# Kernel tuning notes

Measured on AMD Instinct MI355X. Metric: run time of the kernel, lower is better.

Reference implementation:

```python
import jax, jax.numpy as jnp
import numpy as np

N_NODES = 50000   # num graph nodes
N_EDGES = 800000  # avg degree 16
D = 96            # in_channels == out_channels (residual aggr_out + x)


def setup_inputs() -> dict:
    key = jax.random.key(0)
    k0, k1, k2, k3, k4 = jax.random.split(key, 5)
    x = jax.random.normal(k0, (N_NODES, D), dtype=jnp.float32)
    edge_index = jax.random.randint(k1, (2, N_EDGES), 0, N_NODES)  # [2,E]: row0=src(j), row1=dst(i)
    edge_weight = jax.random.uniform(k2, (N_EDGES,), dtype=jnp.float32)
    pagerank = jax.random.uniform(k3, (N_NODES,), dtype=jnp.float32)
    # nn.Linear(in_channels, out_channels) params
    W = jax.random.normal(k4, (D, D), dtype=jnp.float32) / np.sqrt(D).astype(np.float32)
    b = jnp.zeros((D,), dtype=jnp.float32)
    return {"x": x, "edge_index": edge_index, "edge_weight": edge_weight,
            "pagerank": pagerank, "W": W, "b": b}


def reference(x, edge_index, edge_weight, pagerank, W, b):
    # CGCConv (PyG MessagePassing, aggr='add', flow source_to_target):
    #   message: edge_weight * x_j * pagerank_j   (gather from source nodes)
    #   aggregate: scatter-add to destination nodes
    #   update: Linear(aggr_out + x)
    src = edge_index[0]
    dst = edge_index[1]
    # [E, D] messages: per-edge gather-multiply
    msgs = edge_weight[:, None] * x[src] * pagerank[src][:, None]
    aggr = jax.ops.segment_sum(msgs, dst, num_segments=x.shape[0])  # [N, D]
    return (aggr + x) @ W.T + b
```

## Files before the change

kernel.cpp:

```cpp
#include <hip/hip_runtime.h>


constexpr int NN = 50000;
constexpr int NE = 800000;
constexpr int DD = 96;
constexpr int NB = 196;
constexpr int EPB = 2048;
constexpr int NBLK = (NE + EPB - 1) / EPB;
constexpr int CAPB = 4608;

__device__ inline unsigned short f2bf(float f) {
    unsigned u = __float_as_uint(f);
    return (unsigned short)((u + 0x7FFFu + ((u >> 16) & 1u)) >> 16);
}

__global__ __launch_bounds__(256) void k_cvt(const float4* __restrict__ x4,
                                             ushort4* __restrict__ y16v,
                                             int* __restrict__ cur1) {
    if (blockIdx.x == 0 && threadIdx.x < NB) cur1[threadIdx.x] = 0;
    int i = blockIdx.x * blockDim.x + threadIdx.x;
    if (i < NN * DD / 4) {
        float4 v = x4[i];
        y16v[i] = make_ushort4(f2bf(v.x), f2bf(v.y), f2bf(v.z), f2bf(v.w));
    }
}

__global__ __launch_bounds__(256) void k_binA(const int* __restrict__ src,
                                              const int* __restrict__ dst,
                                              const float* __restrict__ ew,
                                              const float* __restrict__ pr,
                                              int* __restrict__ cur1,
                                              int2* __restrict__ stage) {
    __shared__ int h[NB];
    __shared__ int gb[NB];
    int tid = threadIdx.x;
    for (int i = tid; i < NB; i += 256) h[i] = 0;
    __syncthreads();
    int base = blockIdx.x * EPB;

    int2 ent[8]; int bkt[8]; int lrk[8];
    #pragma unroll
    for (int j = 0; j < 8; j++) {
        int e = base + j * 256 + tid;
        bkt[j] = -1;
        if (e < NE) {
            int d = dst[e];
            int s = src[e];
            float c = ew[e] * pr[s];
            int b = d >> 8;
            bkt[j] = b;
            lrk[j] = atomicAdd(&h[b], 1);
            ent[j] = make_int2(s | ((d & 255) << 16), __float_as_int(c));
        }
    }
    __syncthreads();
    for (int i = tid; i < NB; i += 256)
        gb[i] = h[i] ? atomicAdd(&cur1[i], h[i]) : 0;
    __syncthreads();
    #pragma unroll
    for (int j = 0; j < 8; j++)
        if (bkt[j] >= 0)
            stage[(size_t)bkt[j] * CAPB + gb[bkt[j]] + lrk[j]] = ent[j];
}

__global__ __launch_bounds__(512) void k_sortB(int2* __restrict__ stage,
                                               const int* __restrict__ cur1,
                                               int* __restrict__ offs,
                                               int* __restrict__ counts) {
    __shared__ int h[256];
    __shared__ int sc[256];
    __shared__ int2 sorted[CAPB];
    int b = blockIdx.x;
    int tid = threadIdx.x;
    size_t base = (size_t)b * CAPB;
    int n = cur1[b];

    for (int i = tid; i < 256; i += 512) h[i] = 0;
    __syncthreads();

    int2 ent[9]; int lrk[9];
    int m = 0;
    for (int i = tid; i < n; i += 512) {
        int2 e = stage[base + i];
        int dloc = (e.x >> 16) & 0xff;
        lrk[m] = atomicAdd(&h[dloc], 1);
        ent[m] = e;
        m++;
    }
    __syncthreads();
    if (tid < 256) sc[tid] = h[tid];
    __syncthreads();
    #pragma unroll
    for (int o = 1; o < 256; o <<= 1) {
        int t = 0;
        if (tid < 256 && tid >= o) t = sc[tid - o];
        __syncthreads();
        if (tid < 256) sc[tid] += t;
        __syncthreads();
    }
    m = 0;
    for (int i = tid; i < n; i += 512) {
        int2 e = ent[m];
        int dloc = (e.x >> 16) & 0xff;
        sorted[sc[dloc] - h[dloc] + lrk[m]] = e;
        m++;
    }
    __syncthreads();
    for (int i = tid; i < n; i += 512) stage[base + i] = sorted[i];
    if (tid < 256) {
        int d = (b << 8) + tid;
        if (d < NN) {
            offs[d] = (int)base + sc[tid] - h[tid];
            counts[d] = h[tid];
        }
    }
}

__global__ __launch_bounds__(256) void k_pull(const ushort4* __restrict__ y16v,
                                              const float4* __restrict__ x4,
                                              const int* __restrict__ offs,
                                              const int* __restrict__ counts,
                                              const int2* __restrict__ ep,
                                              float4* __restrict__ out4) {
    int g = blockIdx.x * 8 + (threadIdx.x >> 5);
    int lane = threadIdx.x & 31;
    if (g >= NN || lane >= 24) return;
    int beg = offs[g];
    int deg = counts[g];
    float ax = 0.f, ay = 0.f, az = 0.f, aw = 0.f;
    int k = 0;
    for (; k + 4 <= deg; k += 4) {
        int2 e0 = ep[beg + k];
        int2 e1 = ep[beg + k + 1];
        int2 e2 = ep[beg + k + 2];
        int2 e3 = ep[beg + k + 3];
        ushort4 u0 = y16v[(size_t)(e0.x & 0xffff) * 24 + lane];
        ushort4 u1 = y16v[(size_t)(e1.x & 0xffff) * 24 + lane];
        ushort4 u2 = y16v[(size_t)(e2.x & 0xffff) * 24 + lane];
        ushort4 u3 = y16v[(size_t)(e3.x & 0xffff) * 24 + lane];
        float c0 = __int_as_float(e0.y), c1 = __int_as_float(e1.y);
        float c2 = __int_as_float(e2.y), c3 = __int_as_float(e3.y);
        ax += c0 * __uint_as_float((unsigned)u0.x << 16)
            + c1 * __uint_as_float((unsigned)u1.x << 16)
            + c2 * __uint_as_float((unsigned)u2.x << 16)
            + c3 * __uint_as_float((unsigned)u3.x << 16);
        ay += c0 * __uint_as_float((unsigned)u0.y << 16)
            + c1 * __uint_as_float((unsigned)u1.y << 16)
            + c2 * __uint_as_float((unsigned)u2.y << 16)
            + c3 * __uint_as_float((unsigned)u3.y << 16);
        az += c0 * __uint_as_float((unsigned)u0.z << 16)
            + c1 * __uint_as_float((unsigned)u1.z << 16)
            + c2 * __uint_as_float((unsigned)u2.z << 16)
            + c3 * __uint_as_float((unsigned)u3.z << 16);
        aw += c0 * __uint_as_float((unsigned)u0.w << 16)
            + c1 * __uint_as_float((unsigned)u1.w << 16)
            + c2 * __uint_as_float((unsigned)u2.w << 16)
            + c3 * __uint_as_float((unsigned)u3.w << 16);
    }
    for (; k < deg; k++) {
        int2 e = ep[beg + k];
        ushort4 u = y16v[(size_t)(e.x & 0xffff) * 24 + lane];
        float c = __int_as_float(e.y);
        ax += c * __uint_as_float((unsigned)u.x << 16);
        ay += c * __uint_as_float((unsigned)u.y << 16);
        az += c * __uint_as_float((unsigned)u.z << 16);
        aw += c * __uint_as_float((unsigned)u.w << 16);
    }
    float4 xn = x4[(size_t)g * 24 + lane];
    out4[(size_t)g * 24 + lane] = make_float4(ax + xn.x, ay + xn.y,
                                              az + xn.z, aw + xn.w);
}

constexpr int SWS = 100;
__global__ __launch_bounds__(256, 4) void k_gemm(float* __restrict__ io,
                                                 const float* __restrict__ W,
                                                 const float* __restrict__ b) {
    __shared__ float sWt[DD * SWS];
    int tid = threadIdx.x;
    for (int i = tid; i < DD * DD; i += 256) {
        int o = i / DD, d = i - o * DD;
        sWt[d * SWS + o] = W[i];
    }
    __syncthreads();

    int wave = tid >> 6, lane = tid & 63;
    int og = lane & 7, rgl = lane >> 3;
    int o0 = og * 12;
    int rbase = blockIdx.x * 128 + wave * 32 + rgl;
    const float4* io4 = (const float4*)io;

    int r[4];
    #pragma unroll
    for (int t = 0; t < 4; t++) {
        int rr = rbase + 8 * t;
        r[t] = (rr < NN) ? rr : (NN - 1);
    }

    float acc[4][12];
    #pragma unroll
    for (int t = 0; t < 4; t++)
        #pragma unroll
        for (int m = 0; m < 12; m++) acc[t][m] = 0.f;

    for (int d4 = 0; d4 < 24; d4++) {
        float4 xv[4];
        #pragma unroll
        for (int t = 0; t < 4; t++) xv[t] = io4[(size_t)r[t] * 24 + d4];
        #pragma unroll
        for (int dj = 0; dj < 4; dj++) {
            const float* wp = &sWt[(d4 * 4 + dj) * SWS + o0];
            float4 w0 = *(const float4*)(wp);
            float4 w1 = *(const float4*)(wp + 4);
            float4 w2 = *(const float4*)(wp + 8);
            #pragma unroll
            for (int t = 0; t < 4; t++) {
                float xs = (dj == 0) ? xv[t].x : (dj == 1) ? xv[t].y
                         : (dj == 2) ? xv[t].z : xv[t].w;
                acc[t][0]  += xs * w0.x;  acc[t][1]  += xs * w0.y;
                acc[t][2]  += xs * w0.z;  acc[t][3]  += xs * w0.w;
                acc[t][4]  += xs * w1.x;  acc[t][5]  += xs * w1.y;
                acc[t][6]  += xs * w1.z;  acc[t][7]  += xs * w1.w;
                acc[t][8]  += xs * w2.x;  acc[t][9]  += xs * w2.y;
                acc[t][10] += xs * w2.z;  acc[t][11] += xs * w2.w;
            }
        }
    }

    float4 b0 = *(const float4*)(b + o0);
    float4 b1 = *(const float4*)(b + o0 + 4);
    float4 b2 = *(const float4*)(b + o0 + 8);
    float4* io4w = (float4*)io;
    #pragma unroll
    for (int t = 0; t < 4; t++) {
        int rr = rbase + 8 * t;
        if (rr < NN) {
            size_t base = (size_t)rr * 24 + og * 3;
            io4w[base + 0] = make_float4(acc[t][0] + b0.x, acc[t][1] + b0.y,
                                         acc[t][2] + b0.z, acc[t][3] + b0.w);
            io4w[base + 1] = make_float4(acc[t][4] + b1.x, acc[t][5] + b1.y,
                                         acc[t][6] + b1.z, acc[t][7] + b1.w);
            io4w[base + 2] = make_float4(acc[t][8] + b2.x, acc[t][9] + b2.y,
                                         acc[t][10] + b2.z, acc[t][11] + b2.w);
        }
    }
}

extern "C" void kernel_launch(void* const* d_in, const int* in_sizes, int n_in,
                              void* d_out, int out_size, void* d_ws, size_t ws_size,
                              hipStream_t stream) {
    const float* x  = (const float*)d_in[0];
    const int*   ei = (const int*)d_in[1];
    const float* ew = (const float*)d_in[2];
    const float* pr = (const float*)d_in[3];
    const float* W  = (const float*)d_in[4];
    const float* b  = (const float*)d_in[5];
    float* out = (float*)d_out;

    int2* stage = (int2*)d_ws;
    unsigned short* y16 = (unsigned short*)(stage + (size_t)NB * CAPB);
    int* cur1   = (int*)(y16 + (size_t)NN * DD);
    int* offs   = cur1 + NB;
    int* counts = offs + NN;

    const int* src = ei;
    const int* dst = ei + NE;

    int n4 = NN * DD / 4;
    k_cvt<<<(n4 + 255) / 256, 256, 0, stream>>>((const float4*)x, (ushort4*)y16, cur1);
    k_binA<<<NBLK, 256, 0, stream>>>(src, dst, ew, pr, cur1, stage);
    k_sortB<<<NB, 512, 0, stream>>>(stage, cur1, offs, counts);
    k_pull<<<(NN + 7) / 8, 256, 0, stream>>>((const ushort4*)y16, (const float4*)x,
                                             offs, counts, stage, (float4*)out);
    k_gemm<<<(NN + 127) / 128, 256, 0, stream>>>(out, W, b);
}
```

Before: 166.6 us.

## Fuse bucket sort with neighbor pull and merge bf16 convert into binning

Bucket width drops from 256 to 128 destination nodes, so each per-bucket sort can keep its sorted edges in shared memory and do the gather-accumulate directly from there. This removes the write-back of sorted edges, the offs/counts arrays and one kernel launch. The x-to-bf16 conversion now runs in extra blocks of the binning kernel, and a tiny zeroing kernel resets the counters. The cost is that the pull phase runs on only 391 blocks, each with 8 wave groups of 64 lanes (48 active), which may leave the GPU under-occupied and serialize the gather latency.

```diff
diff --git a/kernel.cpp b/kernel.cpp
--- a/kernel.cpp
+++ b/kernel.cpp
@@ -4,57 +4,63 @@
 constexpr int NN = 50000;
 constexpr int NE = 800000;
 constexpr int DD = 96;
-constexpr int NB = 196;
-constexpr int EPB = 2048;
+constexpr int NB = 391;
+constexpr int CAPB = 2432;
+constexpr int EPB = 4096;
 constexpr int NBLK = (NE + EPB - 1) / EPB;
-constexpr int CAPB = 4608;
+constexpr int NCVT = (NN * DD / 4 + 511) / 512;
 
 __device__ inline unsigned short f2bf(float f) {
     unsigned u = __float_as_uint(f);
     return (unsigned short)((u + 0x7FFFu + ((u >> 16) & 1u)) >> 16);
 }
-
-__global__ __launch_bounds__(256) void k_cvt(const float4* __restrict__ x4,
-                                             ushort4* __restrict__ y16v,
-                                             int* __restrict__ cur1) {
-    if (blockIdx.x == 0 && threadIdx.x < NB) cur1[threadIdx.x] = 0;
-    int i = blockIdx.x * blockDim.x + threadIdx.x;
-    if (i < NN * DD / 4) {
-        float4 v = x4[i];
-        y16v[i] = make_ushort4(f2bf(v.x), f2bf(v.y), f2bf(v.z), f2bf(v.w));
-    }
-}
-
-__global__ __launch_bounds__(256) void k_binA(const int* __restrict__ src,
+__device__ inline float bfh(unsigned short v) {
+    return __uint_as_float((unsigned)v << 16);
+}
+
+__global__ __launch_bounds__(512) void k_zero(int* __restrict__ cur1) {
+    if (threadIdx.x < NB) cur1[threadIdx.x] = 0;
+}
+
+__global__ __launch_bounds__(512) void k_prep(const int* __restrict__ src,
                                               const int* __restrict__ dst,
                                               const float* __restrict__ ew,
                                               const float* __restrict__ pr,
                                               int* __restrict__ cur1,
-                                              int2* __restrict__ stage) {
+                                              int2* __restrict__ stage,
+                                              const float4* __restrict__ x4,
+                                              ushort4* __restrict__ y16v) {
+    int tid = threadIdx.x;
+    if (blockIdx.x >= NBLK) {
+        int i = (blockIdx.x - NBLK) * 512 + tid;
+        if (i < NN * DD / 4) {
+            float4 v = x4[i];
+            y16v[i] = make_ushort4(f2bf(v.x), f2bf(v.y), f2bf(v.z), f2bf(v.w));
+        }
+        return;
+    }
     __shared__ int h[NB];
     __shared__ int gb[NB];
-    int tid = threadIdx.x;
-    for (int i = tid; i < NB; i += 256) h[i] = 0;
+    for (int i = tid; i < NB; i += 512) h[i] = 0;
     __syncthreads();
     int base = blockIdx.x * EPB;
 
     int2 ent[8]; int bkt[8]; int lrk[8];
     #pragma unroll
     for (int j = 0; j < 8; j++) {
-        int e = base + j * 256 + tid;
+        int e = base + j * 512 + tid;
         bkt[j] = -1;
         if (e < NE) {
             int d = dst[e];
             int s = src[e];
             float c = ew[e] * pr[s];
-            int b = d >> 8;
-            bkt[j] = b;
-            lrk[j] = atomicAdd(&h[b], 1);
-            ent[j] = make_int2(s | ((d & 255) << 16), __float_as_int(c));
-        }
-    }
-    __syncthreads();
-    for (int i = tid; i < NB; i += 256)
+            bkt[j] = d >> 7;
+            lrk[j] = atomicAdd(&h[d >> 7], 1);
+            ent[j] = make_int2(s | ((d & 127) << 16), __float_as_int(c));
+        }
+    }
+    __syncthreads();
+    for (int i = tid; i < NB; i += 512)
         gb[i] = h[i] ? atomicAdd(&cur1[i], h[i]) : 0;
     __syncthreads();
     #pragma unroll
@@ -63,112 +69,85 @@
             stage[(size_t)bkt[j] * CAPB + gb[bkt[j]] + lrk[j]] = ent[j];
 }
 
-__global__ __launch_bounds__(512) void k_sortB(int2* __restrict__ stage,
-                                               const int* __restrict__ cur1,
-                                               int* __restrict__ offs,
-                                               int* __restrict__ counts) {
-    __shared__ int h[256];
-    __shared__ int sc[256];
-    __shared__ int2 sorted[CAPB];
-    int b = blockIdx.x;
-    int tid = threadIdx.x;
+__global__ __launch_bounds__(512) void k_sortpull(const int2* __restrict__ stage,
+                                                  const int* __restrict__ cur1,
+                                                  const ushort2* __restrict__ y2,
+                                                  const float2* __restrict__ x2,
+                                                  float2* __restrict__ out2) {
+    __shared__ int2 es[CAPB];
+    __shared__ int h[128];
+    __shared__ int sc[128];
+    int b = blockIdx.x, tid = threadIdx.x;
     size_t base = (size_t)b * CAPB;
     int n = cur1[b];
 
-    for (int i = tid; i < 256; i += 512) h[i] = 0;
-    __syncthreads();
-
-    int2 ent[9]; int lrk[9];
+    if (tid < 128) h[tid] = 0;
+    __syncthreads();
+    int2 ent[5]; int lrk[5];
     int m = 0;
     for (int i = tid; i < n; i += 512) {
         int2 e = stage[base + i];
-        int dloc = (e.x >> 16) & 0xff;
-        lrk[m] = atomicAdd(&h[dloc], 1);
-        ent[m] = e;
-        m++;
-    }
-    __syncthreads();
-    if (tid < 256) sc[tid] = h[tid];
-    __syncthreads();
-    #pragma unroll
-    for (int o = 1; o < 256; o <<= 1) {
+        lrk[m] = atomicAdd(&h[(e.x >> 16) & 127], 1);
+        ent[m] = e; m++;
+    }
+    __syncthreads();
+    if (tid < 128) sc[tid] = h[tid];
+    __syncthreads();
+    #pragma unroll
+    for (int o = 1; o < 128; o <<= 1) {
         int t = 0;
-        if (tid < 256 && tid >= o) t = sc[tid - o];
+        if (tid < 128 && tid >= o) t = sc[tid - o];
         __syncthreads();
-        if (tid < 256) sc[tid] += t;
+        if (tid < 128) sc[tid] += t;
         __syncthreads();
     }
     m = 0;
     for (int i = tid; i < n; i += 512) {
         int2 e = ent[m];
-        int dloc = (e.x >> 16) & 0xff;
-        sorted[sc[dloc] - h[dloc] + lrk[m]] = e;
+        int dl = (e.x >> 16) & 127;
+        es[sc[dl] - h[dl] + lrk[m]] = e;
         m++;
     }
     __syncthreads();
-    for (int i = tid; i < n; i += 512) stage[base + i] = sorted[i];
-    if (tid < 256) {
-        int d = (b << 8) + tid;
-        if (d < NN) {
-            offs[d] = (int)base + sc[tid] - h[tid];
-            counts[d] = h[tid];
-        }
-    }
-}
-
-__global__ __launch_bounds__(256) void k_pull(const ushort4* __restrict__ y16v,
-                                              const float4* __restrict__ x4,
-                                              const int* __restrict__ offs,
-                                              const int* __restrict__ counts,
-                                              const int2* __restrict__ ep,
-                                              float4* __restrict__ out4) {
-    int g = blockIdx.x * 8 + (threadIdx.x >> 5);
-    int lane = threadIdx.x & 31;
-    if (g >= NN || lane >= 24) return;
-    int beg = offs[g];
-    int deg = counts[g];
-    float ax = 0.f, ay = 0.f, az = 0.f, aw = 0.f;
-    int k = 0;
-    for (; k + 4 <= deg; k += 4) {
-        int2 e0 = ep[beg + k];
-        int2 e1 = ep[beg + k + 1];
-        int2 e2 = ep[beg + k + 2];
-        int2 e3 = ep[beg + k + 3];
-        ushort4 u0 = y16v[(size_t)(e0.x & 0xffff) * 24 + lane];
-        ushort4 u1 = y16v[(size_t)(e1.x & 0xffff) * 24 + lane];
-        ushort4 u2 = y16v[(size_t)(e2.x & 0xffff) * 24 + lane];
-        ushort4 u3 = y16v[(size_t)(e3.x & 0xffff) * 24 + lane];
-        float c0 = __int_as_float(e0.y), c1 = __int_as_float(e1.y);
-        float c2 = __int_as_float(e2.y), c3 = __int_as_float(e3.y);
-        ax += c0 * __uint_as_float((unsigned)u0.x << 16)
-            + c1 * __uint_as_float((unsigned)u1.x << 16)
-            + c2 * __uint_as_float((unsigned)u2.x << 16)
-            + c3 * __uint_as_float((unsigned)u3.x << 16);
-        ay += c0 * __uint_as_float((unsigned)u0.y << 16)
-            + c1 * __uint_as_float((unsigned)u1.y << 16)
-            + c2 * __uint_as_float((unsigned)u2.y << 16)
-            + c3 * __uint_as_float((unsigned)u3.y << 16);
-        az += c0 * __uint_as_float((unsigned)u0.z << 16)
-            + c1 * __uint_as_float((unsigned)u1.z << 16)
-            + c2 * __uint_as_float((unsigned)u2.z << 16)
-            + c3 * __uint_as_float((unsigned)u3.z << 16);
-        aw += c0 * __uint_as_float((unsigned)u0.w << 16)
-            + c1 * __uint_as_float((unsigned)u1.w << 16)
-            + c2 * __uint_as_float((unsigned)u2.w << 16)
-            + c3 * __uint_as_float((unsigned)u3.w << 16);
-    }
-    for (; k < deg; k++) {
-        int2 e = ep[beg + k];
-        ushort4 u = y16v[(size_t)(e.x & 0xffff) * 24 + lane];
-        float c = __int_as_float(e.y);
-        ax += c * __uint_as_float((unsigned)u.x << 16);
-        ay += c * __uint_as_float((unsigned)u.y << 16);
-        az += c * __uint_as_float((unsigned)u.z << 16);
-        aw += c * __uint_as_float((unsigned)u.w << 16);
-    }
-    float4 xn = x4[(size_t)g * 24 + lane];
-    out4[(size_t)g * 24 + lane] = make_float4(ax + xn.x, ay + xn.y,
-                                              az + xn.z, aw + xn.w);
+
+    int grp = tid >> 6, lane = tid & 63;
+    for (int ni = grp; ni < 128; ni += 8) {
+        int d = (b << 7) + ni;
+        if (d >= NN) break;
+        int beg = sc[ni] - h[ni];
+        int deg = h[ni];
+        float a0 = 0.f, a1 = 0.f;
+        int k = 0;
+        for (; k + 4 <= deg; k += 4) {
+            int2 e0 = es[beg + k],     e1 = es[beg + k + 1];
+            int2 e2 = es[beg + k + 2], e3 = es[beg + k + 3];
+            if (lane < 48) {
+                ushort2 u0 = y2[(size_t)(e0.x & 0xffff) * 48 + lane];
+                ushort2 u1 = y2[(size_t)(e1.x & 0xffff) * 48 + lane];
+                ushort2 u2 = y2[(size_t)(e2.x & 0xffff) * 48 + lane];
+                ushort2 u3 = y2[(size_t)(e3.x & 0xffff) * 48 + lane];
+                float c0 = __int_as_float(e0.y), c1 = __int_as_float(e1.y);
+                float c2 = __int_as_float(e2.y), c3 = __int_as_float(e3.y);
+                a0 += c0 * bfh(u0.x) + c1 * bfh(u1.x)
+                    + c2 * bfh(u2.x) + c3 * bfh(u3.x);
+                a1 += c0 * bfh(u0.y) + c1 * bfh(u1.y)
+                    + c2 * bfh(u2.y) + c3 * bfh(u3.y);
+            }
+        }
+        for (; k < deg; k++) {
+            int2 e = es[beg + k];
+            if (lane < 48) {
+                ushort2 u = y2[(size_t)(e.x & 0xffff) * 48 + lane];
+                float c = __int_as_float(e.y);
+                a0 += c * bfh(u.x);
+                a1 += c * bfh(u.y);
+            }
+        }
+        if (lane < 48) {
+            float2 xv = x2[(size_t)d * 48 + lane];
+            out2[(size_t)d * 48 + lane] = make_float2(a0 + xv.x, a1 + xv.y);
+        }
+    }
 }
 
 constexpr int SWS = 100;
@@ -258,18 +237,15 @@
 
     int2* stage = (int2*)d_ws;
     unsigned short* y16 = (unsigned short*)(stage + (size_t)NB * CAPB);
-    int* cur1   = (int*)(y16 + (size_t)NN * DD);
-    int* offs   = cur1 + NB;
-    int* counts = offs + NN;
+    int* cur1 = (int*)(y16 + (size_t)NN * DD);
 
     const int* src = ei;
     const int* dst = ei + NE;
 
-    int n4 = NN * DD / 4;
-    k_cvt<<<(n4 + 255) / 256, 256, 0, stream>>>((const float4*)x, (ushort4*)y16, cur1);
-    k_binA<<<NBLK, 256, 0, stream>>>(src, dst, ew, pr, cur1, stage);
-    k_sortB<<<NB, 512, 0, stream>>>(stage, cur1, offs, counts);
-    k_pull<<<(NN + 7) / 8, 256, 0, stream>>>((const ushort4*)y16, (const float4*)x,
-                                             offs, counts, stage, (float4*)out);
+    k_zero<<<1, 512, 0, stream>>>(cur1);
+    k_prep<<<NBLK + NCVT, 512, 0, stream>>>(src, dst, ew, pr, cur1, stage,
+                                            (const float4*)x, (ushort4*)y16);
+    k_sortpull<<<NB, 512, 0, stream>>>(stage, cur1, (const ushort2*)y16,
+                                       (const float2*)x, (float2*)out);
     k_gemm<<<(NN + 127) / 128, 256, 0, stream>>>(out, W, b);
 }
```

Result: slower. 194.4 us (+16.7%).

## Fuse bf16 conversion into binning kernel, add nontemporal edge traffic and deeper pull unroll

Applied to the files above, without the earlier changes.

The separate x-to-bf16 conversion kernel is merged into the binning kernel as extra blocks, with a tiny kernel now zeroing the bucket counters. Binning blocks grow to 512 threads and 4096 edges each. Edge records become 64-bit words moved with nontemporal loads and stores. The pull loop gains an 8-way unrolled path that issues more independent gathers in flight. The goal is fewer launch gaps, less cache pollution from the streamed edge data, and more memory-level parallelism, at the cost of higher register use and an extra tiny launch.

```diff
diff --git a/kernel.cpp b/kernel.cpp
--- a/kernel.cpp
+++ b/kernel.cpp
@@ -5,71 +5,82 @@
 constexpr int NE = 800000;
 constexpr int DD = 96;
 constexpr int NB = 196;
-constexpr int EPB = 2048;
+constexpr int CAPB = 4608;
+constexpr int EPB = 4096;
 constexpr int NBLK = (NE + EPB - 1) / EPB;
-constexpr int CAPB = 4608;
+constexpr int NCVT = (NN * DD / 4 + 511) / 512;
 
 __device__ inline unsigned short f2bf(float f) {
     unsigned u = __float_as_uint(f);
     return (unsigned short)((u + 0x7FFFu + ((u >> 16) & 1u)) >> 16);
 }
-
-__global__ __launch_bounds__(256) void k_cvt(const float4* __restrict__ x4,
-                                             ushort4* __restrict__ y16v,
-                                             int* __restrict__ cur1) {
-    if (blockIdx.x == 0 && threadIdx.x < NB) cur1[threadIdx.x] = 0;
-    int i = blockIdx.x * blockDim.x + threadIdx.x;
-    if (i < NN * DD / 4) {
-        float4 v = x4[i];
-        y16v[i] = make_ushort4(f2bf(v.x), f2bf(v.y), f2bf(v.z), f2bf(v.w));
-    }
-}
-
-__global__ __launch_bounds__(256) void k_binA(const int* __restrict__ src,
+__device__ inline float bfh(unsigned short v) {
+    return __uint_as_float((unsigned)v << 16);
+}
+__device__ inline unsigned long long pack_e(int meta, float c) {
+    return (unsigned long long)(unsigned)meta |
+           ((unsigned long long)(unsigned)__float_as_uint(c) << 32);
+}
+
+__global__ __launch_bounds__(256) void k_zero(int* __restrict__ cur1) {
+    if (threadIdx.x < NB) cur1[threadIdx.x] = 0;
+}
+
+__global__ __launch_bounds__(512) void k_prep(const int* __restrict__ src,
                                               const int* __restrict__ dst,
                                               const float* __restrict__ ew,
                                               const float* __restrict__ pr,
                                               int* __restrict__ cur1,
-                                              int2* __restrict__ stage) {
+                                              unsigned long long* __restrict__ stage,
+                                              const float4* __restrict__ x4,
+                                              ushort4* __restrict__ y16v) {
+    int tid = threadIdx.x;
+    if (blockIdx.x >= NBLK) {
+        int i = (blockIdx.x - NBLK) * 512 + tid;
+        if (i < NN * DD / 4) {
+            float4 v = x4[i];
+            y16v[i] = make_ushort4(f2bf(v.x), f2bf(v.y), f2bf(v.z), f2bf(v.w));
+        }
+        return;
+    }
     __shared__ int h[NB];
     __shared__ int gb[NB];
-    int tid = threadIdx.x;
-    for (int i = tid; i < NB; i += 256) h[i] = 0;
+    for (int i = tid; i < NB; i += 512) h[i] = 0;
     __syncthreads();
     int base = blockIdx.x * EPB;
 
-    int2 ent[8]; int bkt[8]; int lrk[8];
+    unsigned long long ent[8]; int bkt[8]; int lrk[8];
     #pragma unroll
     for (int j = 0; j < 8; j++) {
-        int e = base + j * 256 + tid;
+        int e = base + j * 512 + tid;
         bkt[j] = -1;
         if (e < NE) {
             int d = dst[e];
             int s = src[e];
             float c = ew[e] * pr[s];
-            int b = d >> 8;
-            bkt[j] = b;
-            lrk[j] = atomicAdd(&h[b], 1);
-            ent[j] = make_int2(s | ((d & 255) << 16), __float_as_int(c));
-        }
-    }
-    __syncthreads();
-    for (int i = tid; i < NB; i += 256)
+            bkt[j] = d >> 8;
+            lrk[j] = atomicAdd(&h[d >> 8], 1);
+            ent[j] = pack_e(s | ((d & 255) << 16), c);
+        }
+    }
+    __syncthreads();
+    for (int i = tid; i < NB; i += 512)
         gb[i] = h[i] ? atomicAdd(&cur1[i], h[i]) : 0;
     __syncthreads();
     #pragma unroll
     for (int j = 0; j < 8; j++)
         if (bkt[j] >= 0)
-            stage[(size_t)bkt[j] * CAPB + gb[bkt[j]] + lrk[j]] = ent[j];
-}
-
-__global__ __launch_bounds__(512) void k_sortB(int2* __restrict__ stage,
+            __builtin_nontemporal_store(
+                ent[j], &stage[(size_t)bkt[j] * CAPB + gb[bkt[j]] + lrk[j]]);
+}
+
+__global__ __launch_bounds__(512) void k_sortB(unsigned long long* __restrict__ stage,
                                                const int* __restrict__ cur1,
                                                int* __restrict__ offs,
                                                int* __restrict__ counts) {
     __shared__ int h[256];
     __shared__ int sc[256];
-    __shared__ int2 sorted[CAPB];
+    __shared__ unsigned long long sorted[CAPB];
     int b = blockIdx.x;
     int tid = threadIdx.x;
     size_t base = (size_t)b * CAPB;
@@ -78,11 +89,11 @@
     for (int i = tid; i < 256; i += 512) h[i] = 0;
     __syncthreads();
 
-    int2 ent[9]; int lrk[9];
+    unsigned long long ent[9]; int lrk[9];
     int m = 0;
     for (int i = tid; i < n; i += 512) {
-        int2 e = stage[base + i];
-        int dloc = (e.x >> 16) & 0xff;
+        unsigned long long e = __builtin_nontemporal_load(&stage[base + i]);
+        int dloc = ((int)e >> 16) & 0xff;
         lrk[m] = atomicAdd(&h[dloc], 1);
         ent[m] = e;
         m++;
@@ -100,13 +111,14 @@
     }
     m = 0;
     for (int i = tid; i < n; i += 512) {
-        int2 e = ent[m];
-        int dloc = (e.x >> 16) & 0xff;
+        unsigned long long e = ent[m];
+        int dloc = ((int)e >> 16) & 0xff;
         sorted[sc[dloc] - h[dloc] + lrk[m]] = e;
         m++;
     }
     __syncthreads();
-    for (int i = tid; i < n; i += 512) stage[base + i] = sorted[i];
+    for (int i = tid; i < n; i += 512)
+        __builtin_nontemporal_store(sorted[i], &stage[base + i]);
     if (tid < 256) {
         int d = (b << 8) + tid;
         if (d < NN) {
@@ -120,7 +132,7 @@
                                               const float4* __restrict__ x4,
                                               const int* __restrict__ offs,
                                               const int* __restrict__ counts,
-                                              const int2* __restrict__ ep,
+                                              const unsigned long long* __restrict__ ep,
                                               float4* __restrict__ out4) {
     int g = blockIdx.x * 8 + (threadIdx.x >> 5);
     int lane = threadIdx.x & 31;
@@ -129,42 +141,50 @@
     int deg = counts[g];
     float ax = 0.f, ay = 0.f, az = 0.f, aw = 0.f;
     int k = 0;
+    for (; k + 8 <= deg; k += 8) {
+        unsigned long long e[8];
+        #pragma unroll
+        for (int j = 0; j < 8; j++)
+            e[j] = __builtin_nontemporal_load(&ep[beg + k + j]);
+        ushort4 u[8];
+        #pragma unroll
+        for (int j = 0; j < 8; j++)
+            u[j] = y16v[(size_t)((unsigned)e[j] & 0xffff) * 24 + lane];
+        #pragma unroll
+        for (int j = 0; j < 8; j++) {
+            float c = __uint_as_float((unsigned)(e[j] >> 32));
+            ax += c * bfh(u[j].x);
+            ay += c * bfh(u[j].y);
+            az += c * bfh(u[j].z);
+            aw += c * bfh(u[j].w);
+        }
+    }
     for (; k + 4 <= deg; k += 4) {
-        int2 e0 = ep[beg + k];
-        int2 e1 = ep[beg + k + 1];
-        int2 e2 = ep[beg + k + 2];
-        int2 e3 = ep[beg + k + 3];
-        ushort4 u0 = y16v[(size_t)(e0.x & 0xffff) * 24 + lane];
-        ushort4 u1 = y16v[(size_t)(e1.x & 0xffff) * 24 + lane];
-        ushort4 u2 = y16v[(size_t)(e2.x & 0xffff) * 24 + lane];
-        ushort4 u3 = y16v[(size_t)(e3.x & 0xffff) * 24 + lane];
-        float c0 = __int_as_float(e0.y), c1 = __int_as_float(e1.y);
-        float c2 = __int_as_float(e2.y), c3 = __int_as_float(e3.y);
-        ax += c0 * __uint_as_float((unsigned)u0.x << 16)
-            + c1 * __uint_as_float((unsigned)u1.x << 16)
-            + c2 * __uint_as_float((unsigned)u2.x << 16)
-            + c3 * __uint_as_float((unsigned)u3.x << 16);
-        ay += c0 * __uint_as_float((unsigned)u0.y << 16)
-            + c1 * __uint_as_float((unsigned)u1.y << 16)
-            + c2 * __uint_as_float((unsigned)u2.y << 16)
-            + c3 * __uint_as_float((unsigned)u3.y << 16);
-        az += c0 * __uint_as_float((unsigned)u0.z << 16)
-            + c1 * __uint_as_float((unsigned)u1.z << 16)
-            + c2 * __uint_as_float((unsigned)u2.z << 16)
-            + c3 * __uint_as_float((unsigned)u3.z << 16);
-        aw += c0 * __uint_as_float((unsigned)u0.w << 16)
-            + c1 * __uint_as_float((unsigned)u1.w << 16)
-            + c2 * __uint_as_float((unsigned)u2.w << 16)
-            + c3 * __uint_as_float((unsigned)u3.w << 16);
+        unsigned long long e[4];
+        #pragma unroll
+        for (int j = 0; j < 4; j++)
+            e[j] = __builtin_nontemporal_load(&ep[beg + k + j]);
+        ushort4 u[4];
+        #pragma unroll
+        for (int j = 0; j < 4; j++)
+            u[j] = y16v[(size_t)((unsigned)e[j] & 0xffff) * 24 + lane];
+        #pragma unroll
+        for (int j = 0; j < 4; j++) {
+            float c = __uint_as_float((unsigned)(e[j] >> 32));
+            ax += c * bfh(u[j].x);
+            ay += c * bfh(u[j].y);
+            az += c * bfh(u[j].z);
+            aw += c * bfh(u[j].w);
+        }
     }
     for (; k < deg; k++) {
-        int2 e = ep[beg + k];
-        ushort4 u = y16v[(size_t)(e.x & 0xffff) * 24 + lane];
-        float c = __int_as_float(e.y);
-        ax += c * __uint_as_float((unsigned)u.x << 16);
-        ay += c * __uint_as_float((unsigned)u.y << 16);
-        az += c * __uint_as_float((unsigned)u.z << 16);
-        aw += c * __uint_as_float((unsigned)u.w << 16);
+        unsigned long long e = __builtin_nontemporal_load(&ep[beg + k]);
+        ushort4 u = y16v[(size_t)((unsigned)e & 0xffff) * 24 + lane];
+        float c = __uint_as_float((unsigned)(e >> 32));
+        ax += c * bfh(u.x);
+        ay += c * bfh(u.y);
+        az += c * bfh(u.z);
+        aw += c * bfh(u.w);
     }
     float4 xn = x4[(size_t)g * 24 + lane];
     out4[(size_t)g * 24 + lane] = make_float4(ax + xn.x, ay + xn.y,
@@ -256,7 +276,7 @@
     const float* b  = (const float*)d_in[5];
     float* out = (float*)d_out;
 
-    int2* stage = (int2*)d_ws;
+    unsigned long long* stage = (unsigned long long*)d_ws;
     unsigned short* y16 = (unsigned short*)(stage + (size_t)NB * CAPB);
     int* cur1   = (int*)(y16 + (size_t)NN * DD);
     int* offs   = cur1 + NB;
@@ -265,9 +285,9 @@
     const int* src = ei;
     const int* dst = ei + NE;
 
-    int n4 = NN * DD / 4;
-    k_cvt<<<(n4 + 255) / 256, 256, 0, stream>>>((const float4*)x, (ushort4*)y16, cur1);
-    k_binA<<<NBLK, 256, 0, stream>>>(src, dst, ew, pr, cur1, stage);
+    k_zero<<<1, 256, 0, stream>>>(cur1);
+    k_prep<<<NBLK + NCVT, 512, 0, stream>>>(src, dst, ew, pr, cur1, stage,
+                                            (const float4*)x, (ushort4*)y16);
     k_sortB<<<NB, 512, 0, stream>>>(stage, cur1, offs, counts);
     k_pull<<<(NN + 7) / 8, 256, 0, stream>>>((const ushort4*)y16, (const float4*)x,
                                              offs, counts, stage, (float4*)out);
```

Measured after the change: 179.6 us. 1.08x slower.
